# Kernel tuning notes

Measured on AMD Instinct MI355X. Metric: run time of the kernel, lower is better.

## Reference

```python
import jax, jax.numpy as jnp
import numpy as np

B, S, H = 64, 1024, 512
EPS = 1e-5


def layer_norm(x, g, b):
    mu = jnp.mean(x, axis=-1, keepdims=True)
    var = jnp.mean(jnp.square(x - mu), axis=-1, keepdims=True)
    return (x - mu) * jax.lax.rsqrt(var + EPS) * g + b


def lstm(x, w_ih, w_hh, b_ih, b_hh):
    # x: [B,S,H]; gates order (PyTorch): i, f, g, o; w_*: [4H, H]
    gx = jnp.einsum('bsh,gh->bsg', x, w_ih) + b_ih + b_hh  # [B,S,4H] one big GEMM
    gx = jnp.swapaxes(gx, 0, 1)  # time-major [S,B,4H]
    h0 = jnp.zeros((x.shape[0], w_hh.shape[1]), x.dtype)

    def step(carry, g_t):
        h, c = carry
        g = g_t + h @ w_hh.T
        i, f, gg, o = jnp.split(g, 4, axis=-1)
        c = jax.nn.sigmoid(f) * c + jax.nn.sigmoid(i) * jnp.tanh(gg)
        h = jax.nn.sigmoid(o) * jnp.tanh(c)
        return (h, c), h

    _, hs = jax.lax.scan(step, (h0, h0), gx)
    return jnp.swapaxes(hs, 0, 1)  # [B,S,H]


def setup_inputs() -> dict:
    key = jax.random.key(0)
    ks = jax.random.split(key, 12)
    s = 1.0 / np.sqrt(H)  # matches torch default uniform(-1/sqrt(H), 1/sqrt(H)) scale
    return {
        'x': jax.random.normal(ks[0], (B, S, H), jnp.float32),
        'pre_g': jnp.ones((H,), jnp.float32),
        'pre_b': jnp.zeros((H,), jnp.float32),
        'w_ih': jax.random.uniform(ks[1], (4 * H, H), jnp.float32, -s, s),
        'w_hh': jax.random.uniform(ks[2], (4 * H, H), jnp.float32, -s, s),
        'b_ih': jax.random.uniform(ks[3], (4 * H,), jnp.float32, -s, s),
        'b_hh': jax.random.uniform(ks[4], (4 * H,), jnp.float32, -s, s),
        'post_g': jnp.ones((H,), jnp.float32),
        'post_b': jnp.zeros((H,), jnp.float32),
        'w1': jax.random.uniform(ks[5], (H, 2 * H), jnp.float32, -s, s),
        'b1': jax.random.uniform(ks[6], (2 * H,), jnp.float32, -s, s),
        'w2': jax.random.uniform(ks[7], (2 * H, H), jnp.float32, -1.0 / np.sqrt(2 * H), 1.0 / np.sqrt(2 * H)),
        'b2': jax.random.uniform(ks[8], (H,), jnp.float32, -1.0 / np.sqrt(2 * H), 1.0 / np.sqrt(2 * H)),
    }


def reference(x, pre_g, pre_b, w_ih, w_hh, b_ih, b_hh, post_g, post_b, w1, b1, w2, b2):
    # Dropout is identity in eval mode.
    r = lstm(layer_norm(x, pre_g, pre_b), w_ih, w_hh, b_ih, b_hh)
    x = x + r
    h = layer_norm(x, post_g, post_b)
    h = jax.nn.gelu(h @ w1 + b1, approximate=False) @ w2 + b2
    return x + h
```

## Files before the change

### kernel.cpp

```cpp
#include <hip/hip_runtime.h>

typedef unsigned short u16;
typedef unsigned int   u32;
typedef unsigned long long u64;
typedef __attribute__((ext_vector_type(4))) float f32x4;
typedef __attribute__((ext_vector_type(8))) short short8;
typedef __attribute__((ext_vector_type(8))) __bf16 bf16x8v;
typedef __attribute__((ext_vector_type(4))) u32 u32x4;

__device__ __forceinline__ float bf2f(u16 v) { return __uint_as_float(((u32)v) << 16); }
__device__ __forceinline__ u16 f2bf(float f) {
    u32 u = __float_as_uint(f);
    u32 r = (u + 0x7fffu + ((u >> 16) & 1u)) >> 16;
    return (u16)r;
}
__device__ __forceinline__ float sigm(float x) { return 1.f / (1.f + __expf(-x)); }
__device__ __forceinline__ float tanh_f(float x) { return 1.f - 2.f / (__expf(2.f * x) + 1.f); }

template <class A>
__device__ __forceinline__ auto try_mfma(A a, A b, f32x4 c, int)
    -> decltype(__builtin_amdgcn_mfma_f32_16x16x32_bf16(a, b, c, 0, 0, 0)) {
    return __builtin_amdgcn_mfma_f32_16x16x32_bf16(a, b, c, 0, 0, 0);
}
template <class A>
__device__ __forceinline__ f32x4 try_mfma(A a, A b, f32x4 c, long) {
    return __builtin_amdgcn_mfma_f32_16x16x32_bf16(
        __builtin_bit_cast(bf16x8v, a), __builtin_bit_cast(bf16x8v, b), c, 0, 0, 0);
}
__device__ __forceinline__ f32x4 MFMA(short8 a, short8 b, f32x4 c) { return try_mfma(a, b, c, 0); }

__device__ __forceinline__ void cload4(const u32* p0, const u32* p1, const u32* p2, const u32* p3,
                                       u32x4& a, u32x4& b, u32x4& c, u32x4& d) {
    asm volatile("global_load_dwordx4 %0, %4, off sc0 sc1\n\t"
                 "global_load_dwordx4 %1, %5, off sc0 sc1\n\t"
                 "global_load_dwordx4 %2, %6, off sc0 sc1\n\t"
                 "global_load_dwordx4 %3, %7, off sc0 sc1\n\t"
                 "s_waitcnt vmcnt(0)"
                 : "=&v"(a), "=&v"(b), "=&v"(c), "=&v"(d)
                 : "v"(p0), "v"(p1), "v"(p2), "v"(p3)
                 : "memory");
}
__device__ __forceinline__ void cstore1(u32* p, u32 v) {
    asm volatile("global_store_dword %0, %1, off sc0 sc1" :: "v"(p), "v"(v) : "memory");
}


__global__ void k_prep(const float* __restrict__ w_ih, const float* __restrict__ w_hh,
                       const float* __restrict__ b_ih, const float* __restrict__ b_hh,
                       const float* __restrict__ w1, const float* __restrict__ w2,
                       u16* __restrict__ wihb, u16* __restrict__ whhb,
                       u16* __restrict__ w1t, u16* __restrict__ w2t, float* __restrict__ biasc) {
    for (u32 i = blockIdx.x * blockDim.x + threadIdx.x; i < 3147776u; i += gridDim.x * blockDim.x) {
        if (i < 1048576u) { wihb[i] = f2bf(w_ih[i]); }
        else if (i < 2097152u) { u32 j = i - 1048576u; whhb[j] = f2bf(w_hh[j]); }
        else if (i < 2621440u) { u32 j = i - 2097152u; u32 n = j >> 9,  k = j & 511u;  w1t[j] = f2bf(w1[k * 1024u + n]); }
        else if (i < 3145728u) { u32 j = i - 2621440u; u32 n = j >> 10, k = j & 1023u; w2t[j] = f2bf(w2[k * 512u + n]); }
        else { u32 j = i - 3145728u; biasc[j] = b_ih[j] + b_hh[j]; }
    }
}

__global__ void k_init(u32* __restrict__ h_ex) {
    u32 i = blockIdx.x * blockDim.x + threadIdx.x;
    if (i < 65536u) h_ex[i] = 0u;
}

__global__ __launch_bounds__(256) void k_pre_ln(const float* __restrict__ x,
                                                const float* __restrict__ g, const float* __restrict__ b,
                                                u16* __restrict__ out) {
    const int row = blockIdx.x * 4 + (threadIdx.x >> 6);
    const int lane = threadIdx.x & 63;
    const float* xr = x + (size_t)row * 512 + lane * 8;
    float v[8];
    *(float4*)(v)     = *(const float4*)(xr);
    *(float4*)(v + 4) = *(const float4*)(xr + 4);
    float s = 0.f, q = 0.f;
#pragma unroll
    for (int e = 0; e < 8; ++e) { s += v[e]; q += v[e] * v[e]; }
#pragma unroll
    for (int o = 32; o; o >>= 1) { s += __shfl_xor(s, o); q += __shfl_xor(q, o); }
    float mu = s * (1.f / 512.f);
    float rs = rsqrtf(q * (1.f / 512.f) - mu * mu + 1e-5f);
    short8 ov;
#pragma unroll
    for (int e = 0; e < 8; ++e) {
        int cidx = lane * 8 + e;
        ov[e] = (short)f2bf((v[e] - mu) * rs * g[cidx] + b[cidx]);
    }
    *(short8*)(out + (size_t)row * 512 + lane * 8) = ov;
}

__global__ __launch_bounds__(256) void k_res_ln(const float* __restrict__ x, const u16* __restrict__ r,
                                                const float* __restrict__ g, const float* __restrict__ b,
                                                u16* __restrict__ out) {
    const int row = blockIdx.x * 4 + (threadIdx.x >> 6);
    const int lane = threadIdx.x & 63;
    const float* xr = x + (size_t)row * 512 + lane * 8;
    short8 rv = *(const short8*)(r + (size_t)row * 512 + lane * 8);
    float v[8];
    *(float4*)(v)     = *(const float4*)(xr);
    *(float4*)(v + 4) = *(const float4*)(xr + 4);
#pragma unroll
    for (int e = 0; e < 8; ++e) v[e] += bf2f((u16)rv[e]);
    float s = 0.f, q = 0.f;
#pragma unroll
    for (int e = 0; e < 8; ++e) { s += v[e]; q += v[e] * v[e]; }
#pragma unroll
    for (int o = 32; o; o >>= 1) { s += __shfl_xor(s, o); q += __shfl_xor(q, o); }
    float mu = s * (1.f / 512.f);
    float rs = rsqrtf(q * (1.f / 512.f) - mu * mu + 1e-5f);
    short8 ov;
#pragma unroll
    for (int e = 0; e < 8; ++e) {
        int cidx = lane * 8 + e;
        ov[e] = (short)f2bf((v[e] - mu) * rs * g[cidx] + b[cidx]);
    }
    *(short8*)(out + (size_t)row * 512 + lane * 8) = ov;
}

template <int KD, int EPI>
__global__ __launch_bounds__(256, 2)
void k_gemm(const u16* __restrict__ A, const u16* __restrict__ B,
            const float* __restrict__ bias, u16* __restrict__ Cb, float* __restrict__ Cf,
            const float* __restrict__ Xres, const u16* __restrict__ Rres, int N) {
    __shared__ __align__(16) u16 At[128 * 64];
    __shared__ __align__(16) u16 Bt[128 * 64];
    const int tid = threadIdx.x;
    const int lane = tid & 63, wv = tid >> 6;
    const int m0 = blockIdx.y << 7, n0 = blockIdx.x << 7;
    const int wm = (wv >> 1) << 6, wn = (wv & 1) << 6;
    f32x4 acc[4][4] = {};
    const int rr = tid >> 3, kb = tid & 7;
    const int ksw = (kb ^ (rr & 7)) * 8;
    const int wvb = wv * 512;

    for (int k0 = 0; k0 < KD; k0 += 64) {
#pragma unroll
        for (int r = 0; r < 4; ++r) {
            const u16* sa = A + (size_t)(m0 + r * 32 + rr) * KD + (k0 + ksw);
            const u16* sb = B + (size_t)(n0 + r * 32 + rr) * KD + (k0 + ksw);
            __builtin_amdgcn_global_load_lds((const u32*)sa, (u32*)&At[r * 2048 + wvb], 16, 0, 0);
            __builtin_amdgcn_global_load_lds((const u32*)sb, (u32*)&Bt[r * 2048 + wvb], 16, 0, 0);
        }
        __syncthreads();
#pragma unroll
        for (int ks = 0; ks < 2; ++ks) {
            short8 af[4], bf[4];
#pragma unroll
            for (int mt = 0; mt < 4; ++mt) {
                int rowa = wm + mt * 16 + (lane & 15);
                int kba = ((lane >> 4) * 16 + ks * 64) ^ ((rowa & 7) << 4);
                af[mt] = *(const short8*)((const char*)At + rowa * 128 + kba);
                int rowb = wn + mt * 16 + (lane & 15);
                int kbb = ((lane >> 4) * 16 + ks * 64) ^ ((rowb & 7) << 4);
                bf[mt] = *(const short8*)((const char*)Bt + rowb * 128 + kbb);
            }
#pragma unroll
            for (int mt = 0; mt < 4; ++mt)
#pragma unroll
                for (int nt = 0; nt < 4; ++nt)
                    acc[mt][nt] = MFMA(af[mt], bf[nt], acc[mt][nt]);
        }
        __syncthreads();
    }
#pragma unroll
    for (int mt = 0; mt < 4; ++mt) {
#pragma unroll
        for (int nt = 0; nt < 4; ++nt) {
            int gn = n0 + wn + nt * 16 + (lane & 15);
            float bi = bias[gn];
#pragma unroll
            for (int i = 0; i < 4; ++i) {
                int gm = m0 + wm + mt * 16 + (lane >> 4) * 4 + i;
                float v = acc[mt][nt][i] + bi;
                size_t idx = (size_t)gm * (size_t)N + gn;
                if constexpr (EPI == 0) {
                    Cb[idx] = f2bf(v);
                } else if constexpr (EPI == 1) {
                    v = 0.5f * v * (1.f + erff(v * 0.70710678118f));
                    Cb[idx] = f2bf(v);
                } else {
                    Cf[idx] = v + Xres[idx] + bf2f(Rres[idx]);
                }
            }
        }
    }
}

__global__ __launch_bounds__(512, 1)
void k_scan(const u16* __restrict__ gx, const u16* __restrict__ whh,
            u16* __restrict__ rout, u32* __restrict__ h_ex) {
    const int grp = blockIdx.x >> 4, sl = blockIdx.x & 15;
    const int tid = threadIdx.x;
    const int lane = tid & 63, wv = tid >> 6;
    const int gt = wv >> 1, jb = wv & 1;
    const int cb = gt * 512 + sl * 32 + jb * 16;

    __shared__ __align__(16) u16 h_lds[16 * 512];
    __shared__ float g_buf[128 * 17];

    short8 wf[16];
    {
        const u16* wp = whh + (size_t)(cb + (lane & 15)) * 512 + (lane >> 4) * 8;
#pragma unroll
        for (int ks = 0; ks < 16; ++ks) wf[ks] = *(const short8*)(wp + ks * 32);
    }
    const int b_own = tid >> 5, jj = tid & 31;
    float cst = 0.f;
    u32* hex_g = h_ex + (u32)grp * 16384u;
    const int lc = gt * 32 + jb * 16 + (lane & 15);
    const int ngl = cb + (lane & 15);
    const u32 pub_idx = (u32)(b_own * 512 + sl * 32 + jj);

    const int jbyte = (tid & 127) * 8;
    char* ldst[4];
#pragma unroll
    for (int q = 0; q < 4; ++q) {
        int bq = q * 4 + (tid >> 7);
        ldst[q] = (char*)h_lds + bq * 1024 + (jbyte ^ ((bq & 7) << 4));
    }
    const u16* gx_me = gx;
    size_t gx_off[4];
#pragma unroll
    for (int i = 0; i < 4; ++i) {
        int bg = grp * 16 + (lane >> 4) * 4 + i;
        gx_off[i] = (size_t)bg * 1024 * 2048 + ngl;
    }

    u16 gxA[4], gxB[4];
#pragma unroll
    for (int i = 0; i < 4; ++i) gxA[i] = gx_me[gx_off[i]];

    auto step = [&](int t, u16 (&cur)[4], u16 (&nxt)[4]) {
        const u32* bse = hex_g + (u32)(t & 1) * 8192u + tid * 4;
        u32x4 qa, qb, qc, qd;
        int tries = 0;
        for (;;) {
            cload4(bse, bse + 2048, bse + 4096, bse + 6144, qa, qb, qc, qd);
            u32 bad = 0;
#pragma unroll
            for (int e = 0; e < 4; ++e) {
                bad |= (qa[e] >> 16) ^ (u32)t;
                bad |= (qb[e] >> 16) ^ (u32)t;
                bad |= (qc[e] >> 16) ^ (u32)t;
                bad |= (qd[e] >> 16) ^ (u32)t;
            }
            if (!bad) break;
            if (tries++) __builtin_amdgcn_s_sleep(1);
        }
        {
            u32 a0 = (qa[0] & 0xffffu) | (qa[1] << 16), a1 = (qa[2] & 0xffffu) | (qa[3] << 16);
            u32 b0 = (qb[0] & 0xffffu) | (qb[1] << 16), b1 = (qb[2] & 0xffffu) | (qb[3] << 16);
            u32 c0 = (qc[0] & 0xffffu) | (qc[1] << 16), c1 = (qc[2] & 0xffffu) | (qc[3] << 16);
            u32 d0 = (qd[0] & 0xffffu) | (qd[1] << 16), d1 = (qd[2] & 0xffffu) | (qd[3] << 16);
            *(u64*)ldst[0] = (u64)a0 | ((u64)a1 << 32);
            *(u64*)ldst[1] = (u64)b0 | ((u64)b1 << 32);
            *(u64*)ldst[2] = (u64)c0 | ((u64)c1 << 32);
            *(u64*)ldst[3] = (u64)d0 | ((u64)d1 << 32);
        }
        {
            const u16* gp = gx_me + (size_t)(((t + 1) & 1023) * 2048);
#pragma unroll
            for (int i = 0; i < 4; ++i) nxt[i] = gp[gx_off[i]];
        }
        __syncthreads();
        f32x4 a0 = {}, a1 = {}, a2 = {}, a3 = {};
        {
            const int rowa = lane & 15;
            const int kb0 = (lane >> 4) * 16;
            const int sw = (rowa & 7) << 4;
            const char* rb_ = (const char*)h_lds + rowa * 1024;
#pragma unroll
            for (int ks = 0; ks < 4; ++ks) {
                a0 = MFMA(*(const short8*)(rb_ + ((kb0 + (4 * ks + 0) * 64) ^ sw)), wf[4 * ks + 0], a0);
                a1 = MFMA(*(const short8*)(rb_ + ((kb0 + (4 * ks + 1) * 64) ^ sw)), wf[4 * ks + 1], a1);
                a2 = MFMA(*(const short8*)(rb_ + ((kb0 + (4 * ks + 2) * 64) ^ sw)), wf[4 * ks + 2], a2);
                a3 = MFMA(*(const short8*)(rb_ + ((kb0 + (4 * ks + 3) * 64) ^ sw)), wf[4 * ks + 3], a3);
            }
        }
        f32x4 acc = (a0 + a1) + (a2 + a3);
#pragma unroll
        for (int i = 0; i < 4; ++i)
            g_buf[lc * 17 + ((lane >> 4) * 4 + i)] = acc[i] + bf2f(cur[i]);
        __syncthreads();
        {
            float iv = g_buf[jj * 17 + b_own];
            float fv = g_buf[(jj + 32) * 17 + b_own];
            float gv = g_buf[(jj + 64) * 17 + b_own];
            float ov = g_buf[(jj + 96) * 17 + b_own];
            cst = sigm(fv) * cst + sigm(iv) * tanh_f(gv);
            float h = sigm(ov) * tanh_f(cst);
            u16 hb = f2bf(h);
            u32* pp = hex_g + (u32)((t + 1) & 1) * 8192u + pub_idx;
            cstore1(pp, ((u32)(t + 1) << 16) | (u32)hb);
            rout[((size_t)(grp * 16 + b_own) * 1024 + t) * 512 + sl * 32 + jj] = hb;
        }
    };

    for (int t = 0; t < 1024; t += 2) {
        step(t, gxA, gxB);
        step(t + 1, gxB, gxA);
    }
}

extern "C" void kernel_launch(void* const* d_in, const int* in_sizes, int n_in,
                              void* d_out, int out_size, void* d_ws, size_t ws_size,
                              hipStream_t stream) {
    const float* x     = (const float*)d_in[0];
    const float* pre_g = (const float*)d_in[1];
    const float* pre_b = (const float*)d_in[2];
    const float* w_ih  = (const float*)d_in[3];
    const float* w_hh  = (const float*)d_in[4];
    const float* b_ih  = (const float*)d_in[5];
    const float* b_hh  = (const float*)d_in[6];
    const float* post_g= (const float*)d_in[7];
    const float* post_b= (const float*)d_in[8];
    const float* w1    = (const float*)d_in[9];
    const float* b1    = (const float*)d_in[10];
    const float* w2    = (const float*)d_in[11];
    const float* b2    = (const float*)d_in[12];
    float* out = (float*)d_out;

    char* p = (char*)d_ws;
    auto carve = [&](size_t bytes) { void* r = (void*)p; p += (bytes + 255) & ~(size_t)255; return r; };
    u16* xln   = (u16*)carve(64ull * 1024 * 512 * 2);
    u16* gxb   = (u16*)carve(64ull * 1024 * 2048 * 2);
    u16* rb    = (u16*)carve(64ull * 1024 * 512 * 2);
    u16* wihb  = (u16*)carve(2048ull * 512 * 2);
    u16* whhb  = (u16*)carve(2048ull * 512 * 2);
    u16* w1t   = (u16*)carve(1024ull * 512 * 2);
    u16* w2t   = (u16*)carve(512ull * 1024 * 2);
    float* biasc = (float*)carve(2048ull * 4);
    u32* h_ex  = (u32*)carve(65536ull * 4);
    u16* ln1 = xln;
    u16* h1  = gxb;

    k_prep<<<3072, 256, 0, stream>>>(w_ih, w_hh, b_ih, b_hh, w1, w2, wihb, whhb, w1t, w2t, biasc);
    k_init<<<256, 256, 0, stream>>>(h_ex);
    k_pre_ln<<<16384, 256, 0, stream>>>(x, pre_g, pre_b, xln);
    k_gemm<512, 0><<<dim3(16, 512), 256, 0, stream>>>(xln, wihb, biasc, gxb, nullptr, nullptr, nullptr, 2048);
    k_scan<<<64, 512, 0, stream>>>(gxb, whhb, rb, h_ex);
    k_res_ln<<<16384, 256, 0, stream>>>(x, rb, post_g, post_b, ln1);
    k_gemm<512, 1><<<dim3(8, 512), 256, 0, stream>>>(ln1, w1t, b1, h1, nullptr, nullptr, nullptr, 1024);
    k_gemm<1024, 2><<<dim3(4, 512), 256, 0, stream>>>(h1, w2t, b2, nullptr, out, x, rb, 512);
}
```

Before: 3.661 ms.

## Interleave two batch groups per scan block to hide cross-block h exchange latency

Each scan block now processes two independent batch groups, A and B, in alternation. While one group's MFMA and gate phases run, the other group's polled hidden-state exchange load and its gx loads are already in flight, using split issue and wait asm with explicit vmcnt counts. The grid is halved to 32 blocks, so the per-block work per step doubles, and this only pays off if the exchange latency was the bottleneck. The manual vmcnt accounting and the asm-tied registers are fragile and could break ordering if the compiler reorders loads.

```diff
diff --git a/kernel.cpp b/kernel.cpp
--- a/kernel.cpp
+++ b/kernel.cpp
@@ -29,20 +29,45 @@
 }
 __device__ __forceinline__ f32x4 MFMA(short8 a, short8 b, f32x4 c) { return try_mfma(a, b, c, 0); }
 
-__device__ __forceinline__ void cload4(const u32* p0, const u32* p1, const u32* p2, const u32* p3,
-                                       u32x4& a, u32x4& b, u32x4& c, u32x4& d) {
+__device__ __forceinline__ void cload4_issue(const u32* p0, const u32* p1, const u32* p2, const u32* p3,
+                                             u32x4& a, u32x4& b, u32x4& c, u32x4& d) {
     asm volatile("global_load_dwordx4 %0, %4, off sc0 sc1\n\t"
                  "global_load_dwordx4 %1, %5, off sc0 sc1\n\t"
                  "global_load_dwordx4 %2, %6, off sc0 sc1\n\t"
-                 "global_load_dwordx4 %3, %7, off sc0 sc1\n\t"
-                 "s_waitcnt vmcnt(0)"
+                 "global_load_dwordx4 %3, %7, off sc0 sc1"
                  : "=&v"(a), "=&v"(b), "=&v"(c), "=&v"(d)
                  : "v"(p0), "v"(p1), "v"(p2), "v"(p3)
                  : "memory");
 }
+__device__ __forceinline__ void gxload4(const u16* p0, const u16* p1, const u16* p2, const u16* p3,
+                                        u32& a, u32& b, u32& c, u32& d) {
+    asm volatile("global_load_ushort %0, %4, off\n\t"
+                 "global_load_ushort %1, %5, off\n\t"
+                 "global_load_ushort %2, %6, off\n\t"
+                 "global_load_ushort %3, %7, off"
+                 : "=&v"(a), "=&v"(b), "=&v"(c), "=&v"(d)
+                 : "v"(p0), "v"(p1), "v"(p2), "v"(p3)
+                 : "memory");
+}
 __device__ __forceinline__ void cstore1(u32* p, u32 v) {
     asm volatile("global_store_dword %0, %1, off sc0 sc1" :: "v"(p), "v"(v) : "memory");
 }
+__device__ __forceinline__ void store_short(u16* p, u32 v) {
+    asm volatile("global_store_short %0, %1, off" :: "v"(p), "v"(v) : "memory");
+}
+
+#define WAITVM_TIE(IMM, a, b, c, d, g0, g1, g2, g3)                                   \
+    do {                                                                              \
+        asm volatile("s_waitcnt vmcnt(" IMM ")"                                       \
+                     : "+v"(a), "+v"(b), "+v"(c), "+v"(d),                            \
+                       "+v"(g0), "+v"(g1), "+v"(g2), "+v"(g3)::"memory");             \
+        __builtin_amdgcn_sched_barrier(0);                                            \
+    } while (0)
+#define WAITVM0(a, b, c, d)                                                           \
+    do {                                                                              \
+        asm volatile("s_waitcnt vmcnt(0)" : "+v"(a), "+v"(b), "+v"(c), "+v"(d)::"memory"); \
+        __builtin_amdgcn_sched_barrier(0);                                            \
+    } while (0)
 
 
 __global__ void k_prep(const float* __restrict__ w_ih, const float* __restrict__ w_hh,
@@ -186,16 +211,83 @@
     }
 }
 
+__device__ __forceinline__ void poll_retry(const u32* bse, u32 t, u32x4& a, u32x4& b, u32x4& c, u32x4& d) {
+    int tries = 0;
+    for (;;) {
+        u32 bad = 0;
+#pragma unroll
+        for (int e = 0; e < 4; ++e) {
+            bad |= (a[e] >> 16) ^ t;
+            bad |= (b[e] >> 16) ^ t;
+            bad |= (c[e] >> 16) ^ t;
+            bad |= (d[e] >> 16) ^ t;
+        }
+        if (!bad) return;
+        if (tries++) __builtin_amdgcn_s_sleep(1);
+        cload4_issue(bse, bse + 2048, bse + 4096, bse + 6144, a, b, c, d);
+        WAITVM0(a, b, c, d);
+    }
+}
+
+__device__ __forceinline__ void lds_pack(u16* hlds, const int* lofs,
+                                         const u32x4& a, const u32x4& b, const u32x4& c, const u32x4& d) {
+    char* base = (char*)hlds;
+    u32 a0 = (a[0] & 0xffffu) | (a[1] << 16), a1 = (a[2] & 0xffffu) | (a[3] << 16);
+    u32 b0 = (b[0] & 0xffffu) | (b[1] << 16), b1 = (b[2] & 0xffffu) | (b[3] << 16);
+    u32 c0 = (c[0] & 0xffffu) | (c[1] << 16), c1 = (c[2] & 0xffffu) | (c[3] << 16);
+    u32 d0 = (d[0] & 0xffffu) | (d[1] << 16), d1 = (d[2] & 0xffffu) | (d[3] << 16);
+    *(u64*)(base + lofs[0]) = (u64)a0 | ((u64)a1 << 32);
+    *(u64*)(base + lofs[1]) = (u64)b0 | ((u64)b1 << 32);
+    *(u64*)(base + lofs[2]) = (u64)c0 | ((u64)c1 << 32);
+    *(u64*)(base + lofs[3]) = (u64)d0 | ((u64)d1 << 32);
+}
+
+__device__ __forceinline__ void mfma_phase(const u16* hlds, const short8* wf, const u32* gxv,
+                                           int lane, int lc, float* g_buf) {
+    f32x4 a0 = {}, a1 = {}, a2 = {}, a3 = {};
+    const int rowa = lane & 15;
+    const int kb0 = (lane >> 4) * 16;
+    const int sw = (rowa & 7) << 4;
+    const char* rb_ = (const char*)hlds + rowa * 1024;
+#pragma unroll
+    for (int ks = 0; ks < 4; ++ks) {
+        a0 = MFMA(*(const short8*)(rb_ + ((kb0 + (4 * ks + 0) * 64) ^ sw)), wf[4 * ks + 0], a0);
+        a1 = MFMA(*(const short8*)(rb_ + ((kb0 + (4 * ks + 1) * 64) ^ sw)), wf[4 * ks + 1], a1);
+        a2 = MFMA(*(const short8*)(rb_ + ((kb0 + (4 * ks + 2) * 64) ^ sw)), wf[4 * ks + 2], a2);
+        a3 = MFMA(*(const short8*)(rb_ + ((kb0 + (4 * ks + 3) * 64) ^ sw)), wf[4 * ks + 3], a3);
+    }
+    f32x4 acc = (a0 + a1) + (a2 + a3);
+#pragma unroll
+    for (int i = 0; i < 4; ++i)
+        g_buf[lc * 17 + ((lane >> 4) * 4 + i)] = acc[i] + bf2f((u16)gxv[i]);
+}
+
+__device__ __forceinline__ void gates_phase(float& cst, const float* g_buf, int b_own, int jj,
+                                            u32* pubp, u16* routp, u32 tag1) {
+    float iv = g_buf[jj * 17 + b_own];
+    float fv = g_buf[(jj + 32) * 17 + b_own];
+    float gv = g_buf[(jj + 64) * 17 + b_own];
+    float ov = g_buf[(jj + 96) * 17 + b_own];
+    cst = sigm(fv) * cst + sigm(iv) * tanh_f(gv);
+    float h = sigm(ov) * tanh_f(cst);
+    u16 hb = f2bf(h);
+    cstore1(pubp, (tag1 << 16) | (u32)hb);
+    store_short(routp, (u32)hb);
+}
+
 __global__ __launch_bounds__(512, 1)
 void k_scan(const u16* __restrict__ gx, const u16* __restrict__ whh,
             u16* __restrict__ rout, u32* __restrict__ h_ex) {
-    const int grp = blockIdx.x >> 4, sl = blockIdx.x & 15;
+    const int sl = blockIdx.x & 15;
+    const int pr = blockIdx.x >> 4;
+    const int gA = pr * 2, gB = pr * 2 + 1;
     const int tid = threadIdx.x;
     const int lane = tid & 63, wv = tid >> 6;
     const int gt = wv >> 1, jb = wv & 1;
     const int cb = gt * 512 + sl * 32 + jb * 16;
 
-    __shared__ __align__(16) u16 h_lds[16 * 512];
+    __shared__ __align__(16) u16 hldsA[16 * 512];
+    __shared__ __align__(16) u16 hldsB[16 * 512];
     __shared__ float g_buf[128 * 17];
 
     short8 wf[16];
@@ -205,100 +297,76 @@
         for (int ks = 0; ks < 16; ++ks) wf[ks] = *(const short8*)(wp + ks * 32);
     }
     const int b_own = tid >> 5, jj = tid & 31;
-    float cst = 0.f;
-    u32* hex_g = h_ex + (u32)grp * 16384u;
+    float cstA = 0.f, cstB = 0.f;
+    u32* hexA = h_ex + (u32)gA * 16384u;
+    u32* hexB = h_ex + (u32)gB * 16384u;
     const int lc = gt * 32 + jb * 16 + (lane & 15);
     const int ngl = cb + (lane & 15);
     const u32 pub_idx = (u32)(b_own * 512 + sl * 32 + jj);
 
     const int jbyte = (tid & 127) * 8;
-    char* ldst[4];
+    int lofs[4];
 #pragma unroll
     for (int q = 0; q < 4; ++q) {
         int bq = q * 4 + (tid >> 7);
-        ldst[q] = (char*)h_lds + bq * 1024 + (jbyte ^ ((bq & 7) << 4));
-    }
-    const u16* gx_me = gx;
-    size_t gx_off[4];
+        lofs[q] = bq * 1024 + (jbyte ^ ((bq & 7) << 4));
+    }
+    const u16 *gpA[4], *gpB[4];
 #pragma unroll
     for (int i = 0; i < 4; ++i) {
-        int bg = grp * 16 + (lane >> 4) * 4 + i;
-        gx_off[i] = (size_t)bg * 1024 * 2048 + ngl;
-    }
-
-    u16 gxA[4], gxB[4];
-#pragma unroll
-    for (int i = 0; i < 4; ++i) gxA[i] = gx_me[gx_off[i]];
-
-    auto step = [&](int t, u16 (&cur)[4], u16 (&nxt)[4]) {
-        const u32* bse = hex_g + (u32)(t & 1) * 8192u + tid * 4;
-        u32x4 qa, qb, qc, qd;
-        int tries = 0;
-        for (;;) {
-            cload4(bse, bse + 2048, bse + 4096, bse + 6144, qa, qb, qc, qd);
-            u32 bad = 0;
-#pragma unroll
-            for (int e = 0; e < 4; ++e) {
-                bad |= (qa[e] >> 16) ^ (u32)t;
-                bad |= (qb[e] >> 16) ^ (u32)t;
-                bad |= (qc[e] >> 16) ^ (u32)t;
-                bad |= (qd[e] >> 16) ^ (u32)t;
-            }
-            if (!bad) break;
-            if (tries++) __builtin_amdgcn_s_sleep(1);
+        int bi = (lane >> 4) * 4 + i;
+        gpA[i] = gx + (size_t)(gA * 16 + bi) * 1024 * 2048 + ngl;
+        gpB[i] = gx + (size_t)(gB * 16 + bi) * 1024 * 2048 + ngl;
+    }
+    u16* rpA = rout + (size_t)(gA * 16 + b_own) * 1024 * 512 + sl * 32 + jj;
+    u16* rpB = rout + (size_t)(gB * 16 + b_own) * 1024 * 512 + sl * 32 + jj;
+
+    u32 gxA[4], gxB[4];
+    u32x4 qa, qb, qc, qd;
+    u32x4 ua, ub, uc, ud;
+
+    gxload4(gpA[0], gpA[1], gpA[2], gpA[3], gxA[0], gxA[1], gxA[2], gxA[3]);
+    {
+        const u32* bse = hexA + tid * 4;
+        cload4_issue(bse, bse + 2048, bse + 4096, bse + 6144, qa, qb, qc, qd);
+    }
+    gxload4(gpB[0], gpB[1], gpB[2], gpB[3], gxB[0], gxB[1], gxB[2], gxB[3]);
+
+    for (u32 t = 0; t < 1024; ++t) {
+        const u32 part = (t & 1) * 8192u;
+        const u32 parn = ((t + 1) & 1) * 8192u;
+        const u32* bA = hexA + part + tid * 4;
+        const u32* bB = hexB + part + tid * 4;
+        const int adv = (t < 1023) ? 2048 : 0;
+
+        if (t == 0) { WAITVM_TIE("4", qa, qb, qc, qd, gxA[0], gxA[1], gxA[2], gxA[3]); }
+        else        { WAITVM_TIE("6", qa, qb, qc, qd, gxA[0], gxA[1], gxA[2], gxA[3]); }
+        poll_retry(bA, t, qa, qb, qc, qd);
+        lds_pack(hldsA, lofs, qa, qb, qc, qd);
+        cload4_issue(bB, bB + 2048, bB + 4096, bB + 6144, ua, ub, uc, ud);
+        __syncthreads();
+        mfma_phase(hldsA, wf, gxA, lane, lc, g_buf);
+#pragma unroll
+        for (int i = 0; i < 4; ++i) gpA[i] += adv;
+        gxload4(gpA[0], gpA[1], gpA[2], gpA[3], gxA[0], gxA[1], gxA[2], gxA[3]);
+        __syncthreads();
+        gates_phase(cstA, g_buf, b_own, jj, hexA + parn + pub_idx, rpA, t + 1);
+        rpA += 512;
+        WAITVM_TIE("6", ua, ub, uc, ud, gxB[0], gxB[1], gxB[2], gxB[3]);
+        poll_retry(bB, t, ua, ub, uc, ud);
+        lds_pack(hldsB, lofs, ua, ub, uc, ud);
+        {
+            const u32* bA2 = hexA + parn + tid * 4;
+            cload4_issue(bA2, bA2 + 2048, bA2 + 4096, bA2 + 6144, qa, qb, qc, qd);
         }
-        {
-            u32 a0 = (qa[0] & 0xffffu) | (qa[1] << 16), a1 = (qa[2] & 0xffffu) | (qa[3] << 16);
-            u32 b0 = (qb[0] & 0xffffu) | (qb[1] << 16), b1 = (qb[2] & 0xffffu) | (qb[3] << 16);
-            u32 c0 = (qc[0] & 0xffffu) | (qc[1] << 16), c1 = (qc[2] & 0xffffu) | (qc[3] << 16);
-            u32 d0 = (qd[0] & 0xffffu) | (qd[1] << 16), d1 = (qd[2] & 0xffffu) | (qd[3] << 16);
-            *(u64*)ldst[0] = (u64)a0 | ((u64)a1 << 32);
-            *(u64*)ldst[1] = (u64)b0 | ((u64)b1 << 32);
-            *(u64*)ldst[2] = (u64)c0 | ((u64)c1 << 32);
-            *(u64*)ldst[3] = (u64)d0 | ((u64)d1 << 32);
-        }
-        {
-            const u16* gp = gx_me + (size_t)(((t + 1) & 1023) * 2048);
-#pragma unroll
-            for (int i = 0; i < 4; ++i) nxt[i] = gp[gx_off[i]];
-        }
-        __syncthreads();
-        f32x4 a0 = {}, a1 = {}, a2 = {}, a3 = {};
-        {
-            const int rowa = lane & 15;
-            const int kb0 = (lane >> 4) * 16;
-            const int sw = (rowa & 7) << 4;
-            const char* rb_ = (const char*)h_lds + rowa * 1024;
-#pragma unroll
-            for (int ks = 0; ks < 4; ++ks) {
-                a0 = MFMA(*(const short8*)(rb_ + ((kb0 + (4 * ks + 0) * 64) ^ sw)), wf[4 * ks + 0], a0);
-                a1 = MFMA(*(const short8*)(rb_ + ((kb0 + (4 * ks + 1) * 64) ^ sw)), wf[4 * ks + 1], a1);
-                a2 = MFMA(*(const short8*)(rb_ + ((kb0 + (4 * ks + 2) * 64) ^ sw)), wf[4 * ks + 2], a2);
-                a3 = MFMA(*(const short8*)(rb_ + ((kb0 + (4 * ks + 3) * 64) ^ sw)), wf[4 * ks + 3], a3);
-            }
-        }
-        f32x4 acc = (a0 + a1) + (a2 + a3);
-#pragma unroll
-        for (int i = 0; i < 4; ++i)
-            g_buf[lc * 17 + ((lane >> 4) * 4 + i)] = acc[i] + bf2f(cur[i]);
-        __syncthreads();
-        {
-            float iv = g_buf[jj * 17 + b_own];
-            float fv = g_buf[(jj + 32) * 17 + b_own];
-            float gv = g_buf[(jj + 64) * 17 + b_own];
-            float ov = g_buf[(jj + 96) * 17 + b_own];
-            cst = sigm(fv) * cst + sigm(iv) * tanh_f(gv);
-            float h = sigm(ov) * tanh_f(cst);
-            u16 hb = f2bf(h);
-            u32* pp = hex_g + (u32)((t + 1) & 1) * 8192u + pub_idx;
-            cstore1(pp, ((u32)(t + 1) << 16) | (u32)hb);
-            rout[((size_t)(grp * 16 + b_own) * 1024 + t) * 512 + sl * 32 + jj] = hb;
-        }
-    };
-
-    for (int t = 0; t < 1024; t += 2) {
-        step(t, gxA, gxB);
-        step(t + 1, gxB, gxA);
+        __syncthreads();
+        mfma_phase(hldsB, wf, gxB, lane, lc, g_buf);
+#pragma unroll
+        for (int i = 0; i < 4; ++i) gpB[i] += adv;
+        gxload4(gpB[0], gpB[1], gpB[2], gpB[3], gxB[0], gxB[1], gxB[2], gxB[3]);
+        __syncthreads();
+        gates_phase(cstB, g_buf, b_own, jj, hexB + parn + pub_idx, rpB, t + 1);
+        rpB += 512;
     }
 }
 
@@ -338,7 +406,7 @@
     k_init<<<256, 256, 0, stream>>>(h_ex);
     k_pre_ln<<<16384, 256, 0, stream>>>(x, pre_g, pre_b, xln);
     k_gemm<512, 0><<<dim3(16, 512), 256, 0, stream>>>(xln, wihb, biasc, gxb, nullptr, nullptr, nullptr, 2048);
-    k_scan<<<64, 512, 0, stream>>>(gxb, whhb, rb, h_ex);
+    k_scan<<<32, 512, 0, stream>>>(gxb, whhb, rb, h_ex);
     k_res_ln<<<16384, 256, 0, stream>>>(x, rb, post_g, post_b, ln1);
     k_gemm<512, 1><<<dim3(8, 512), 256, 0, stream>>>(ln1, w1t, b1, h1, nullptr, nullptr, nullptr, 1024);
     k_gemm<1024, 2><<<dim3(4, 512), 256, 0, stream>>>(h1, w2t, b2, nullptr, out, x, rb, 512);
```

Result: slower. 4.324 ms (+18.1%).

## Restructure LSTM scan into 8 batch groups with fast sc0 polling and mirrored flags

Applied to the files above, without the earlier changes.

The recurrent scan now splits the batch into 8 groups of 8 rows, with 8 slices of 64 hidden units per group, so each block computes twice as many columns and keeps two weight fragment sets in registers. Exchange polling first uses sc0-scoped loads on a primary buffer and falls back to system-scope loads on a mirror copy, which is meant to cut cross-block synchronization latency per timestep. Each block also skips reading back its own slice and writes it straight into LDS. Barriers become raw s_barrier with an lgkmcnt wait. The risks are higher register pressure and reliance on cache-scope behaviour for correctness across XCDs.

```diff
diff --git a/kernel.cpp b/kernel.cpp
--- a/kernel.cpp
+++ b/kernel.cpp
@@ -29,20 +29,33 @@
 }
 __device__ __forceinline__ f32x4 MFMA(short8 a, short8 b, f32x4 c) { return try_mfma(a, b, c, 0); }
 
-__device__ __forceinline__ void cload4(const u32* p0, const u32* p1, const u32* p2, const u32* p3,
-                                       u32x4& a, u32x4& b, u32x4& c, u32x4& d) {
-    asm volatile("global_load_dwordx4 %0, %4, off sc0 sc1\n\t"
-                 "global_load_dwordx4 %1, %5, off sc0 sc1\n\t"
-                 "global_load_dwordx4 %2, %6, off sc0 sc1\n\t"
-                 "global_load_dwordx4 %3, %7, off sc0 sc1\n\t"
+__device__ __forceinline__ void poll_sc0(const u32* p0, const u32* p1, u32x4& a, u32x4& b) {
+    asm volatile("global_load_dwordx4 %0, %2, off sc0\n\t"
+                 "global_load_dwordx4 %1, %3, off sc0\n\t"
                  "s_waitcnt vmcnt(0)"
-                 : "=&v"(a), "=&v"(b), "=&v"(c), "=&v"(d)
-                 : "v"(p0), "v"(p1), "v"(p2), "v"(p3)
-                 : "memory");
-}
-__device__ __forceinline__ void cstore1(u32* p, u32 v) {
+                 : "=&v"(a), "=&v"(b) : "v"(p0), "v"(p1) : "memory");
+}
+__device__ __forceinline__ void poll_sys(const u32* p0, const u32* p1, u32x4& a, u32x4& b) {
+    asm volatile("global_load_dwordx4 %0, %2, off sc0 sc1\n\t"
+                 "global_load_dwordx4 %1, %3, off sc0 sc1\n\t"
+                 "s_waitcnt vmcnt(0)"
+                 : "=&v"(a), "=&v"(b) : "v"(p0), "v"(p1) : "memory");
+}
+__device__ __forceinline__ void cstore_sc0(u32* p, u32 v) {
+    asm volatile("global_store_dword %0, %1, off sc0" :: "v"(p), "v"(v) : "memory");
+}
+__device__ __forceinline__ void cstore_sys(u32* p, u32 v) {
     asm volatile("global_store_dword %0, %1, off sc0 sc1" :: "v"(p), "v"(v) : "memory");
 }
+__device__ __forceinline__ void store_short(u16* p, u32 v) {
+    asm volatile("global_store_short %0, %1, off" :: "v"(p), "v"(v) : "memory");
+}
+
+#define LDS_BARRIER()                                                                 \
+    do {                                                                              \
+        asm volatile("s_waitcnt lgkmcnt(0)\n\ts_barrier" ::: "memory");               \
+        __builtin_amdgcn_sched_barrier(0);                                            \
+    } while (0)
 
 
 __global__ void k_prep(const float* __restrict__ w_ih, const float* __restrict__ w_hh,
@@ -61,7 +74,7 @@
 
 __global__ void k_init(u32* __restrict__ h_ex) {
     u32 i = blockIdx.x * blockDim.x + threadIdx.x;
-    if (i < 65536u) h_ex[i] = 0u;
+    if (i < 131072u) h_ex[i] = 0u;
 }
 
 __global__ __launch_bounds__(256) void k_pre_ln(const float* __restrict__ x,
@@ -189,116 +202,145 @@
 __global__ __launch_bounds__(512, 1)
 void k_scan(const u16* __restrict__ gx, const u16* __restrict__ whh,
             u16* __restrict__ rout, u32* __restrict__ h_ex) {
-    const int grp = blockIdx.x >> 4, sl = blockIdx.x & 15;
+    const int grp = blockIdx.x & 7, sl = blockIdx.x >> 3;
     const int tid = threadIdx.x;
     const int lane = tid & 63, wv = tid >> 6;
-    const int gt = wv >> 1, jb = wv & 1;
-    const int cb = gt * 512 + sl * 32 + jb * 16;
+    const int gt = wv >> 1, jh = (wv & 1) * 32;
+    const int cb0 = gt * 512 + sl * 64 + jh;
 
     __shared__ __align__(16) u16 h_lds[16 * 512];
-    __shared__ float g_buf[128 * 17];
-
-    short8 wf[16];
+    __shared__ float g_buf[256 * 9];
+
+#pragma unroll
+    for (int k = 0; k < 4; ++k) ((u64*)h_lds)[tid + k * 512] = 0ull;
+
+    short8 wf0[16], wf1[16];
     {
-        const u16* wp = whh + (size_t)(cb + (lane & 15)) * 512 + (lane >> 4) * 8;
-#pragma unroll
-        for (int ks = 0; ks < 16; ++ks) wf[ks] = *(const short8*)(wp + ks * 32);
-    }
-    const int b_own = tid >> 5, jj = tid & 31;
+        const u16* wp0 = whh + (size_t)(cb0 + (lane & 15)) * 512 + (lane >> 4) * 8;
+        const u16* wp1 = wp0 + 16 * 512;
+#pragma unroll
+        for (int ks = 0; ks < 16; ++ks) {
+            wf0[ks] = *(const short8*)(wp0 + ks * 32);
+            wf1[ks] = *(const short8*)(wp1 + ks * 32);
+        }
+    }
+
+    const int b_own = tid >> 6, jj = tid & 63;
     float cst = 0.f;
-    u32* hex_g = h_ex + (u32)grp * 16384u;
-    const int lc = gt * 32 + jb * 16 + (lane & 15);
-    const int ngl = cb + (lane & 15);
-    const u32 pub_idx = (u32)(b_own * 512 + sl * 32 + jj);
-
-    const int jbyte = (tid & 127) * 8;
-    char* ldst[4];
-#pragma unroll
-    for (int q = 0; q < 4; ++q) {
+    u32* pprim = h_ex + (u32)grp * 8192u;
+    u32* pmir  = pprim + 65536u;
+    const u32 pub_idx = (u32)(b_own * 512 + sl * 64 + jj);
+    const int s_c = (tid & 127) >> 4;
+    const bool skip = (s_c == sl);
+    const int own_off = b_own * 1024 + (((sl * 64 + jj) * 2) ^ (b_own << 4));
+
+    int lofs[2];
+#pragma unroll
+    for (int q = 0; q < 2; ++q) {
         int bq = q * 4 + (tid >> 7);
-        ldst[q] = (char*)h_lds + bq * 1024 + (jbyte ^ ((bq & 7) << 4));
-    }
-    const u16* gx_me = gx;
-    size_t gx_off[4];
+        lofs[q] = bq * 1024 + (((tid & 127) * 8) ^ ((bq & 7) << 4));
+    }
+    const u16* gpA[4];
+    const u16* gpB[4];
 #pragma unroll
     for (int i = 0; i < 4; ++i) {
-        int bg = grp * 16 + (lane >> 4) * 4 + i;
-        gx_off[i] = (size_t)bg * 1024 * 2048 + ngl;
-    }
-
-    u16 gxA[4], gxB[4];
-#pragma unroll
-    for (int i = 0; i < 4; ++i) gxA[i] = gx_me[gx_off[i]];
-
-    auto step = [&](int t, u16 (&cur)[4], u16 (&nxt)[4]) {
-        const u32* bse = hex_g + (u32)(t & 1) * 8192u + tid * 4;
-        u32x4 qa, qb, qc, qd;
-        int tries = 0;
-        for (;;) {
-            cload4(bse, bse + 2048, bse + 4096, bse + 6144, qa, qb, qc, qd);
-            u32 bad = 0;
-#pragma unroll
-            for (int e = 0; e < 4; ++e) {
-                bad |= (qa[e] >> 16) ^ (u32)t;
-                bad |= (qb[e] >> 16) ^ (u32)t;
-                bad |= (qc[e] >> 16) ^ (u32)t;
-                bad |= (qd[e] >> 16) ^ (u32)t;
-            }
-            if (!bad) break;
-            if (tries++) __builtin_amdgcn_s_sleep(1);
-        }
-        {
+        int bi = ((lane >> 4) & 1) * 4 + i;
+        gpA[i] = gx + (size_t)(grp * 8 + bi) * 1024 * 2048 + cb0 + (lane & 15);
+        gpB[i] = gpA[i] + 2048;
+    }
+    u16* routp = rout + (size_t)(grp * 8 + b_own) * 1024 * 512 + sl * 64 + jj;
+
+    u16 gA[8], gB[8];
+#pragma unroll
+    for (int i = 0; i < 4; ++i) { gA[2 * i] = gpA[i][0]; gA[2 * i + 1] = gpA[i][16]; }
+#pragma unroll
+    for (int i = 0; i < 4; ++i) { gB[2 * i] = gpB[i][0]; gB[2 * i + 1] = gpB[i][16]; }
+
+    __syncthreads();
+
+    auto stepbody = [&](u32 t, u16 (&cur)[8], const u16* (&gp)[4]) {
+        const u32 part = (t & 1) * 4096u;
+        const u32 parn = ((t + 1) & 1) * 4096u;
+        u32x4 qa, qb;
+        if (!skip) {
+            const u32* pp = pprim + part + tid * 4;
+            const u32* pm = pmir + part + tid * 4;
+            int tries = 0;
+            for (;;) {
+                if (tries < 3) poll_sc0(pp, pp + 2048, qa, qb);
+                else           poll_sys(pm, pm + 2048, qa, qb);
+                u32 bad = 0;
+#pragma unroll
+                for (int e = 0; e < 4; ++e) {
+                    bad |= (qa[e] >> 16) ^ t;
+                    bad |= (qb[e] >> 16) ^ t;
+                }
+                if (!bad) break;
+                ++tries;
+                if (tries >= 2) __builtin_amdgcn_s_sleep(1);
+            }
             u32 a0 = (qa[0] & 0xffffu) | (qa[1] << 16), a1 = (qa[2] & 0xffffu) | (qa[3] << 16);
             u32 b0 = (qb[0] & 0xffffu) | (qb[1] << 16), b1 = (qb[2] & 0xffffu) | (qb[3] << 16);
-            u32 c0 = (qc[0] & 0xffffu) | (qc[1] << 16), c1 = (qc[2] & 0xffffu) | (qc[3] << 16);
-            u32 d0 = (qd[0] & 0xffffu) | (qd[1] << 16), d1 = (qd[2] & 0xffffu) | (qd[3] << 16);
-            *(u64*)ldst[0] = (u64)a0 | ((u64)a1 << 32);
-            *(u64*)ldst[1] = (u64)b0 | ((u64)b1 << 32);
-            *(u64*)ldst[2] = (u64)c0 | ((u64)c1 << 32);
-            *(u64*)ldst[3] = (u64)d0 | ((u64)d1 << 32);
-        }
-        {
-            const u16* gp = gx_me + (size_t)(((t + 1) & 1023) * 2048);
-#pragma unroll
-            for (int i = 0; i < 4; ++i) nxt[i] = gp[gx_off[i]];
-        }
-        __syncthreads();
-        f32x4 a0 = {}, a1 = {}, a2 = {}, a3 = {};
+            *(u64*)((char*)h_lds + lofs[0]) = (u64)a0 | ((u64)a1 << 32);
+            *(u64*)((char*)h_lds + lofs[1]) = (u64)b0 | ((u64)b1 << 32);
+        }
+        LDS_BARRIER();
+        f32x4 a00 = {}, a01 = {}, a02 = {}, a03 = {}, a10 = {}, a11 = {}, a12 = {}, a13 = {};
         {
             const int rowa = lane & 15;
             const int kb0 = (lane >> 4) * 16;
             const int sw = (rowa & 7) << 4;
             const char* rb_ = (const char*)h_lds + rowa * 1024;
 #pragma unroll
-            for (int ks = 0; ks < 4; ++ks) {
-                a0 = MFMA(*(const short8*)(rb_ + ((kb0 + (4 * ks + 0) * 64) ^ sw)), wf[4 * ks + 0], a0);
-                a1 = MFMA(*(const short8*)(rb_ + ((kb0 + (4 * ks + 1) * 64) ^ sw)), wf[4 * ks + 1], a1);
-                a2 = MFMA(*(const short8*)(rb_ + ((kb0 + (4 * ks + 2) * 64) ^ sw)), wf[4 * ks + 2], a2);
-                a3 = MFMA(*(const short8*)(rb_ + ((kb0 + (4 * ks + 3) * 64) ^ sw)), wf[4 * ks + 3], a3);
-            }
-        }
-        f32x4 acc = (a0 + a1) + (a2 + a3);
-#pragma unroll
-        for (int i = 0; i < 4; ++i)
-            g_buf[lc * 17 + ((lane >> 4) * 4 + i)] = acc[i] + bf2f(cur[i]);
-        __syncthreads();
+            for (int kk = 0; kk < 4; ++kk) {
+                short8 f0 = *(const short8*)(rb_ + ((kb0 + (4 * kk + 0) * 64) ^ sw));
+                short8 f1 = *(const short8*)(rb_ + ((kb0 + (4 * kk + 1) * 64) ^ sw));
+                short8 f2 = *(const short8*)(rb_ + ((kb0 + (4 * kk + 2) * 64) ^ sw));
+                short8 f3 = *(const short8*)(rb_ + ((kb0 + (4 * kk + 3) * 64) ^ sw));
+                a00 = MFMA(f0, wf0[4 * kk + 0], a00); a10 = MFMA(f0, wf1[4 * kk + 0], a10);
+                a01 = MFMA(f1, wf0[4 * kk + 1], a01); a11 = MFMA(f1, wf1[4 * kk + 1], a11);
+                a02 = MFMA(f2, wf0[4 * kk + 2], a02); a12 = MFMA(f2, wf1[4 * kk + 2], a12);
+                a03 = MFMA(f3, wf0[4 * kk + 3], a03); a13 = MFMA(f3, wf1[4 * kk + 3], a13);
+            }
+        }
+        f32x4 acc0 = (a00 + a01) + (a02 + a03);
+        f32x4 acc1 = (a10 + a11) + (a12 + a13);
+        if ((lane >> 4) < 2) {
+            const int lc0 = gt * 64 + jh + (lane & 15);
+            const int m0 = (lane >> 4) * 4;
+#pragma unroll
+            for (int i = 0; i < 4; ++i) {
+                g_buf[lc0 * 9 + m0 + i]        = acc0[i] + bf2f((u16)cur[2 * i]);
+                g_buf[(lc0 + 16) * 9 + m0 + i] = acc1[i] + bf2f((u16)cur[2 * i + 1]);
+            }
+        }
+        if (t < 1022) {
+#pragma unroll
+            for (int i = 0; i < 4; ++i) gp[i] += 4096;
+        }
+#pragma unroll
+        for (int i = 0; i < 4; ++i) { cur[2 * i] = gp[i][0]; cur[2 * i + 1] = gp[i][16]; }
+        LDS_BARRIER();
         {
-            float iv = g_buf[jj * 17 + b_own];
-            float fv = g_buf[(jj + 32) * 17 + b_own];
-            float gv = g_buf[(jj + 64) * 17 + b_own];
-            float ov = g_buf[(jj + 96) * 17 + b_own];
+            float iv = g_buf[(jj) * 9 + b_own];
+            float fv = g_buf[(jj + 64) * 9 + b_own];
+            float gv = g_buf[(jj + 128) * 9 + b_own];
+            float ov = g_buf[(jj + 192) * 9 + b_own];
             cst = sigm(fv) * cst + sigm(iv) * tanh_f(gv);
             float h = sigm(ov) * tanh_f(cst);
-            u16 hb = f2bf(h);
-            u32* pp = hex_g + (u32)((t + 1) & 1) * 8192u + pub_idx;
-            cstore1(pp, ((u32)(t + 1) << 16) | (u32)hb);
-            rout[((size_t)(grp * 16 + b_own) * 1024 + t) * 512 + sl * 32 + jj] = hb;
+            u32 hb = (u32)f2bf(h);
+            *(u16*)((char*)h_lds + own_off) = (u16)hb;
+            u32 w = ((t + 1) << 16) | hb;
+            cstore_sc0(pprim + parn + pub_idx, w);
+            cstore_sys(pmir + parn + pub_idx, w);
+            store_short(routp, hb);
+            routp += 512;
         }
     };
 
-    for (int t = 0; t < 1024; t += 2) {
-        step(t, gxA, gxB);
-        step(t + 1, gxB, gxA);
+    for (u32 t = 0; t < 1024; t += 2) {
+        stepbody(t, gA, gpA);
+        stepbody(t + 1, gB, gpB);
     }
 }
 
@@ -330,12 +372,12 @@
     u16* w1t   = (u16*)carve(1024ull * 512 * 2);
     u16* w2t   = (u16*)carve(512ull * 1024 * 2);
     float* biasc = (float*)carve(2048ull * 4);
-    u32* h_ex  = (u32*)carve(65536ull * 4);
+    u32* h_ex  = (u32*)carve(131072ull * 4);
     u16* ln1 = xln;
     u16* h1  = gxb;
 
     k_prep<<<3072, 256, 0, stream>>>(w_ih, w_hh, b_ih, b_hh, w1, w2, wihb, whhb, w1t, w2t, biasc);
-    k_init<<<256, 256, 0, stream>>>(h_ex);
+    k_init<<<512, 256, 0, stream>>>(h_ex);
     k_pre_ln<<<16384, 256, 0, stream>>>(x, pre_g, pre_b, xln);
     k_gemm<512, 0><<<dim3(16, 512), 256, 0, stream>>>(xln, wihb, biasc, gxb, nullptr, nullptr, nullptr, 2048);
     k_scan<<<64, 512, 0, stream>>>(gxb, whhb, rb, h_ex);
```

Result: faster. 3.034 ms (-17.1%).
